# Performance work log

Hardware: AMD Instinct MI355X
Metric: run time of the kernel (lower is better)

Reference implementation:

```python
import jax, jax.numpy as jnp
import numpy as np

B, H, W, D = 4, 64, 64, 384
M, P = 12, 9
DH = D // M             # 32 head dim
DFF = 3 * D             # 1152 FFN hidden
N = H * W               # 4096 queries (single level)


def setup_inputs():
    key = jax.random.key(0)
    ks = jax.random.split(key, 12)
    g = lambda k, s, sc=0.02: jax.random.normal(k, s, jnp.float32) * sc
    return {
        "x": jax.random.normal(ks[0], (B, D, H, W), jnp.float32),
        "qry_masks": jnp.zeros((B, H, W), jnp.float32),
        "so_w": g(ks[1], (M * P * 2, D)), "so_b": g(ks[2], (M * P * 2,)),
        "aw_w": g(ks[3], (M * P, D)), "aw_b": g(ks[4], (M * P,)),
        "vp_w": g(ks[5], (D, D)), "vp_b": jnp.zeros((D,), jnp.float32),
        "op_w": g(ks[6], (D, D)), "op_b": jnp.zeros((D,), jnp.float32),
        "ln1_g": jnp.ones((D,), jnp.float32), "ln1_b": jnp.zeros((D,), jnp.float32),
        "w1": g(ks[7], (DFF, D)), "w2": g(ks[8], (D, DFF)),
        "ln2_g": jnp.ones((D,), jnp.float32), "ln2_b": jnp.zeros((D,), jnp.float32),
        "level_embed": g(ks[9], (1, D), 1.0),
    }


def _layernorm(x, g, b, eps=1e-5):
    mu = x.mean(-1, keepdims=True)
    v = ((x - mu) ** 2).mean(-1, keepdims=True)
    return (x - mu) * jax.lax.rsqrt(v + eps) * g + b


def _sine_pos(mask):
    # mask: [B,H,W] bool. mmdet SinePositionalEncoding(num_feats=D//2, normalize=True)
    not_mask = (~mask).astype(jnp.float32)
    y = jnp.cumsum(not_mask, 1)
    x = jnp.cumsum(not_mask, 2)
    eps, scale = 1e-6, 2.0 * np.pi
    y = y / (y[:, -1:, :] + eps) * scale
    x = x / (x[:, :, -1:] + eps) * scale
    nf = D // 2
    dim_t = 10000.0 ** (2.0 * (jnp.arange(nf) // 2).astype(jnp.float32) / nf)
    px, py = x[..., None] / dim_t, y[..., None] / dim_t

    def interleave(p):
        return jnp.stack([jnp.sin(p[..., 0::2]), jnp.cos(p[..., 1::2])], -1).reshape(p.shape[:-1] + (nf,))

    return jnp.concatenate([interleave(py), interleave(px)], -1)  # [B,H,W,D]


def _bilinear_gather(v, px, py):
    # v: [B,M,HW,DH]; px,py: [B,M,NP] pixel coords (grid_sample align_corners=False, zero pad)
    x0 = jnp.floor(px); y0 = jnp.floor(py)
    lx, ly = px - x0, py - y0
    x0i, y0i = x0.astype(jnp.int32), y0.astype(jnp.int32)
    out = jnp.zeros(v.shape[:2] + (px.shape[-1], v.shape[-1]), v.dtype)
    for dx, dy, wgt in ((0, 0, (1 - lx) * (1 - ly)), (1, 0, lx * (1 - ly)),
                        (0, 1, (1 - lx) * ly), (1, 1, lx * ly)):
        xi, yi = x0i + dx, y0i + dy
        valid = ((xi >= 0) & (xi < W) & (yi >= 0) & (yi < H)).astype(v.dtype)
        idx = jnp.clip(yi, 0, H - 1) * W + jnp.clip(xi, 0, W - 1)
        g = jnp.take_along_axis(v, idx[..., None], axis=2)  # [B,M,NP,DH]
        out = out + (wgt * valid)[..., None] * g
    return out


def _msdeform_attn(q, value_in, ref, mask_flat,
                   so_w, so_b, aw_w, aw_b, vp_w, vp_b, op_w, op_b):
    value = value_in @ vp_w.T + vp_b                      # [B,N,D]
    value = jnp.where(mask_flat[..., None], 0.0, value)
    so = (q @ so_w.T + so_b).reshape(B, N, M, P, 2)       # single level
    aw = jax.nn.softmax((q @ aw_w.T + aw_b).reshape(B, N, M, P), axis=-1)
    norm = jnp.array([W, H], jnp.float32)
    loc = ref[:, :, None, None, :] + so / norm            # [B,N,M,P,2] in [0,1]
    v = value.reshape(B, N, M, DH).transpose(0, 2, 1, 3)  # [B,M,HW,DH]
    px = (loc[..., 0] * W - 0.5).transpose(0, 2, 1, 3).reshape(B, M, N * P)
    py = (loc[..., 1] * H - 0.5).transpose(0, 2, 1, 3).reshape(B, M, N * P)
    sampled = _bilinear_gather(v, px, py).reshape(B, M, N, P, DH)
    out = jnp.einsum('bmnpd,bnmp->bnmd', sampled, aw).reshape(B, N, D)
    return out @ op_w.T + op_b


def reference(x, qry_masks, so_w, so_b, aw_w, aw_b, vp_w, vp_b, op_w, op_b,
              ln1_g, ln1_b, w1, w2, ln2_g, ln2_b, level_embed):
    mask = (qry_masks == 255.0)                           # [B,H,W] bool
    pos = _sine_pos(mask).reshape(B, N, D) + level_embed[0]
    src = x.reshape(B, D, N).transpose(0, 2, 1)           # [B,N,D]
    mask_flat = mask.reshape(B, N)
    gy, gx = jnp.meshgrid((jnp.arange(H, dtype=jnp.float32) + 0.5) / H,
                          (jnp.arange(W, dtype=jnp.float32) + 0.5) / W, indexing='ij')
    ref = jnp.stack([gx.reshape(-1), gy.reshape(-1)], -1)[None]  # [1,N,2] (x,y)
    q = src
    attn = _msdeform_attn(q + pos, q, ref, mask_flat,
                          so_w, so_b, aw_w, aw_b, vp_w, vp_b, op_w, op_b)
    q = _layernorm(q + attn, ln1_g, ln1_b)
    q = _layernorm(q + jax.nn.relu(q @ w1.T) @ w2.T, ln2_g, ln2_b)
    return q.transpose(0, 2, 1).reshape(B, D, H, W)
```

## Files before the change

### kernel.cpp

```cpp
#include <hip/hip_runtime.h>
#include <math.h>

#define Bc   4
#define Hc   64
#define Wc   64
#define Dc   384
#define Nc   4096
#define Mc   12
#define Pc   9
#define DHc  32
#define DFFc 1152
#define BNc  (Bc*Nc)

typedef __attribute__((ext_vector_type(8))) short short8;
typedef __attribute__((ext_vector_type(4))) float floatx4;

__device__ __forceinline__ ushort f2bf(float f) {
    union { float f; unsigned u; } v; v.f = f;
    unsigned r = v.u + 0x7fffu + ((v.u >> 16) & 1u);
    return (ushort)(r >> 16);
}
__device__ __forceinline__ float bf2f(ushort u) {
    union { unsigned u; float f; } v; v.u = (unsigned)u << 16; return v.f;
}

__device__ __forceinline__ void gload_lds16(const void* g, void* l) {
    __builtin_amdgcn_global_load_lds(
        (const __attribute__((address_space(1))) void*)(uintptr_t)g,
        (__attribute__((address_space(3))) void*)(uintptr_t)l,
        16, 0, 0);
}

#define SOW_N  82944
#define AWW_N  41472
#define VPW_N  147456
#define OPW_N  147456
#define W1_N   442368
#define W2_N   442368
#define WTOT   1304064

__global__ void init_kernel(const float* __restrict__ so_w,
                            const float* __restrict__ aw_w,
                            const float* __restrict__ vp_w,
                            const float* __restrict__ op_w,
                            const float* __restrict__ w1,
                            const float* __restrict__ w2,
                            const float* __restrict__ so_b,
                            const float* __restrict__ aw_b,
                            const float* __restrict__ qmask,
                            ushort* __restrict__ out,
                            float* __restrict__ bias_out,
                            float* __restrict__ cum_y,
                            float* __restrict__ cum_x) {
    int i = blockIdx.x * 256 + threadIdx.x;
    if (i < WTOT) {
        float v;
        int j = i;
        if (j < SOW_N) v = so_w[j];
        else if ((j -= SOW_N) < AWW_N) v = aw_w[j];
        else if ((j -= AWW_N) < VPW_N) v = vp_w[j];
        else if ((j -= VPW_N) < OPW_N) v = op_w[j];
        else if ((j -= OPW_N) < W1_N)  v = w1[j];
        else { j -= W1_N; v = w2[j]; }
        out[i] = f2bf(v);
        return;
    }
    int j = i - WTOT;
    if (j < 384) {
        bias_out[j] = (j < 216) ? so_b[j] : (j < 324 ? aw_b[j - 216] : 0.f);
        return;
    }
    int t = j - 384;
    if (t < Bc * Wc) {
        int b = t / Wc, w = t % Wc;
        float run = 0.f;
        for (int h = 0; h < Hc; ++h) {
            run += (qmask[(b * Hc + h) * Wc + w] == 255.0f) ? 0.f : 1.f;
            cum_y[(b * Hc + h) * Wc + w] = run;
        }
    } else if (t < Bc * Wc + Bc * Hc) {
        int t2 = t - Bc * Wc;
        int b = t2 / Hc, h = t2 % Hc;
        float run = 0.f;
        for (int w = 0; w < Wc; ++w) {
            run += (qmask[(b * Hc + h) * Wc + w] == 255.0f) ? 0.f : 1.f;
            cum_x[(b * Hc + h) * Wc + w] = run;
        }
    }
}

__global__ void transpose_pos_kernel(const float* __restrict__ x,
                                     const float* __restrict__ cum_y,
                                     const float* __restrict__ cum_x,
                                     const float* __restrict__ level_embed,
                                     ushort* __restrict__ src_bf,
                                     ushort* __restrict__ qpos_bf) {
    __shared__ float tile[32][33];
    int b  = blockIdx.z;
    int n0 = blockIdx.x * 32, d0 = blockIdx.y * 32;
    int tx = threadIdx.x, ty = threadIdx.y;
    tile[ty][tx] = x[((size_t)b * Dc + (d0 + ty)) * Nc + (n0 + tx)];
    __syncthreads();
    int n = n0 + ty, d = d0 + tx;
    float v = tile[tx][ty];
    size_t oi = ((size_t)b * Nc + n) * Dc + d;
    src_bf[oi] = f2bf(v);
    int h = n >> 6, w = n & 63;
    const float TWO_PI = 6.28318530717958647692f;
    float vy = cum_y[(b * Hc + h) * Wc + w] /
               (cum_y[(b * Hc + (Hc - 1)) * Wc + w] + 1e-6f) * TWO_PI;
    float vx = cum_x[(b * Hc + h) * Wc + w] /
               (cum_x[(b * Hc + h) * Wc + (Wc - 1)] + 1e-6f) * TWO_PI;
    int   i  = (d < 192) ? d : d - 192;
    float vv = (d < 192) ? vy : vx;
    float e   = (float)(i >> 1) * (2.0f / 192.0f);
    float idt = exp2f(e * -13.28771237954945f);
    float ang = vv * idt;
    float pe  = (i & 1) ? __cosf(ang) : __sinf(ang);
    qpos_bf[oi] = f2bf(v + pe + level_embed[d]);
}

template <int KT>
__device__ __forceinline__ void gemm_core(
        const ushort* __restrict__ A, const ushort* __restrict__ Wt,
        const float* __restrict__ bias,
        float* __restrict__ Cf, ushort* __restrict__ Cb,
        int Nout, int relu, const float* __restrict__ qmask,
        ushort* As, ushort* Bs) {
    constexpr int NCH = KT / 32;
    const int tid  = threadIdx.x;
    const int m0   = blockIdx.x * 128;
    const int n0   = blockIdx.y * 128;
    const int lane = tid & 63;
    const int wv   = tid >> 6;
    const int wr   = (wv >> 1) * 64;
    const int wc   = (wv & 1) * 64;
    const int quad = lane >> 4;
    const int lrow = lane & 15;
    const int srow = wv * 32 + (lane >> 2);
    const int scol = (lane & 3) * 8;

    floatx4 acc[4][4];
    #pragma unroll
    for (int i = 0; i < 4; ++i)
        #pragma unroll
        for (int j = 0; j < 4; ++j)
            acc[i][j] = (floatx4)(0.f);

    #pragma unroll
    for (int s = 0; s < 2; ++s) {
        gload_lds16(A  + (size_t)(m0 + srow + s * 16) * KT + scol,
                    As + wv * 1024 + s * 512);
        gload_lds16(Wt + (size_t)(n0 + srow + s * 16) * KT + scol,
                    Bs + wv * 1024 + s * 512);
    }

    for (int c = 0; c < NCH; ++c) {
        const int cur = c & 1;
        __syncthreads();
        if (c + 1 < NCH) {
            const int k0 = (c + 1) * 32;
            #pragma unroll
            for (int s = 0; s < 2; ++s) {
                gload_lds16(A  + (size_t)(m0 + srow + s * 16) * KT + k0 + scol,
                            As + (cur ^ 1) * 4096 + wv * 1024 + s * 512);
                gload_lds16(Wt + (size_t)(n0 + srow + s * 16) * KT + k0 + scol,
                            Bs + (cur ^ 1) * 4096 + wv * 1024 + s * 512);
            }
        }
        short8 afr[4], bfr[4];
        #pragma unroll
        for (int i = 0; i < 4; ++i)
            afr[i] = *(const short8*)(As + cur * 4096 +
                                      (wr + i * 16 + lrow) * 32 + quad * 8);
        #pragma unroll
        for (int j = 0; j < 4; ++j)
            bfr[j] = *(const short8*)(Bs + cur * 4096 +
                                      (wc + j * 16 + lrow) * 32 + quad * 8);
        #pragma unroll
        for (int i = 0; i < 4; ++i)
            #pragma unroll
            for (int j = 0; j < 4; ++j)
                acc[i][j] = __builtin_amdgcn_mfma_f32_16x16x32_bf16(
                    afr[i], bfr[j], acc[i][j], 0, 0, 0);
    }

    float mz[4][4];
    #pragma unroll
    for (int i = 0; i < 4; ++i)
        #pragma unroll
        for (int r = 0; r < 4; ++r) {
            int row = m0 + wr + i * 16 + quad * 4 + r;
            mz[i][r] = (qmask && qmask[row] == 255.0f) ? 0.f : 1.f;
        }

    #pragma unroll
    for (int i = 0; i < 4; ++i) {
        #pragma unroll
        for (int j = 0; j < 4; ++j) {
            int col = n0 + wc + j * 16 + lrow;
            if (col >= Nout) continue;
            float bsv = bias ? bias[col] : 0.f;
            #pragma unroll
            for (int r = 0; r < 4; ++r) {
                int row = m0 + wr + i * 16 + quad * 4 + r;
                float v = acc[i][j][r] + bsv;
                if (relu) v = fmaxf(v, 0.f);
                v *= mz[i][r];
                if (Cf) Cf[(size_t)row * Nout + col] = v;
                if (Cb) Cb[(size_t)row * Nout + col] = f2bf(v);
            }
        }
    }
}

template <int KT>
__global__ __launch_bounds__(256) void gemm_single_kernel(
        const ushort* __restrict__ A, const ushort* __restrict__ Wt,
        const float* __restrict__ bias,
        float* __restrict__ Cf, ushort* __restrict__ Cb,
        int Nout, int relu, const float* __restrict__ qmask) {
    __shared__ ushort As[2 * 128 * 32];
    __shared__ ushort Bs[2 * 128 * 32];
    gemm_core<KT>(A, Wt, bias, Cf, Cb, Nout, relu, qmask, As, Bs);
}

__global__ __launch_bounds__(256) void gemm_dual_kernel(
        const ushort* __restrict__ A0, const ushort* __restrict__ W0,
        const float* __restrict__ b0, float* __restrict__ Cf0,
        const ushort* __restrict__ A1, const ushort* __restrict__ W1,
        const float* __restrict__ b1, ushort* __restrict__ Cb1,
        const float* __restrict__ qmask) {
    __shared__ ushort As[2 * 128 * 32];
    __shared__ ushort Bs[2 * 128 * 32];
    if (blockIdx.z == 0)
        gemm_core<384>(A0, W0, b0, Cf0, nullptr, 384, 0, nullptr, As, Bs);
    else
        gemm_core<384>(A1, W1, b1, nullptr, Cb1, 384, 0, qmask, As, Bs);
}

template <int KT, int MODE>
__global__ __launch_bounds__(512) void gemm_fullrow_kernel(
        const ushort* __restrict__ A, const ushort* __restrict__ Wt,
        const float* __restrict__ bias, const void* __restrict__ resid,
        const float* __restrict__ g, const float* __restrict__ beta,
        float* __restrict__ outf, ushort* __restrict__ outb) {
    constexpr int NCH = KT / 32;
    __shared__ ushort smem[28672];
    __shared__ float eps1[8][64], eps2[8][64];
    __shared__ float mu_l[64], rs_l[64];
    ushort* As = smem;
    ushort* Bs = smem + 4096;
    const int tid  = threadIdx.x;
    const int lane = tid & 63;
    const int wv   = tid >> 6;
    const int quad = lane >> 4;
    const int lrow = lane & 15;
    const int m0   = blockIdx.x * 64;
    const int srow = lane >> 2;
    const int scol = (lane & 3) * 8;

    floatx4 acc[4][3];
    #pragma unroll
    for (int i = 0; i < 4; ++i)
        #pragma unroll
        for (int j = 0; j < 3; ++j)
            acc[i][j] = (floatx4)(0.f);

    if (wv < 4)
        gload_lds16(A + (size_t)(m0 + wv * 16 + srow) * KT + scol,
                    As + wv * 512);
    #pragma unroll
    for (int s = 0; s < 3; ++s)
        gload_lds16(Wt + (size_t)(wv * 48 + s * 16 + srow) * KT + scol,
                    Bs + wv * 1536 + s * 512);

    for (int c = 0; c < NCH; ++c) {
        const int cur = c & 1;
        __syncthreads();
        if (c + 1 < NCH) {
            const int k0 = (c + 1) * 32;
            if (wv < 4)
                gload_lds16(A + (size_t)(m0 + wv * 16 + srow) * KT + k0 + scol,
                            As + (cur ^ 1) * 2048 + wv * 512);
            #pragma unroll
            for (int s = 0; s < 3; ++s)
                gload_lds16(Wt + (size_t)(wv * 48 + s * 16 + srow) * KT + k0 + scol,
                            Bs + (cur ^ 1) * 12288 + wv * 1536 + s * 512);
        }
        short8 afr[4], bfr[3];
        #pragma unroll
        for (int i = 0; i < 4; ++i)
            afr[i] = *(const short8*)(As + cur * 2048 +
                                      (i * 16 + lrow) * 32 + quad * 8);
        #pragma unroll
        for (int j = 0; j < 3; ++j)
            bfr[j] = *(const short8*)(Bs + cur * 12288 +
                                      (wv * 48 + j * 16 + lrow) * 32 + quad * 8);
        #pragma unroll
        for (int i = 0; i < 4; ++i)
            #pragma unroll
            for (int j = 0; j < 3; ++j)
                acc[i][j] = __builtin_amdgcn_mfma_f32_16x16x32_bf16(
                    afr[i], bfr[j], acc[i][j], 0, 0, 0);
    }

    float s1[16], s2[16];
    #pragma unroll
    for (int k = 0; k < 16; ++k) { s1[k] = 0.f; s2[k] = 0.f; }
    #pragma unroll
    for (int i = 0; i < 4; ++i) {
        #pragma unroll
        for (int r = 0; r < 4; ++r) {
            int rl = i * 16 + quad * 4 + r;
            #pragma unroll
            for (int j = 0; j < 3; ++j) {
                int col = wv * 48 + j * 16 + lrow;
                float t = acc[i][j][r];
                if (bias) t += bias[col];
                if (MODE == 0)
                    t += bf2f(((const ushort*)resid)[(size_t)(m0 + rl) * Dc + col]);
                else
                    t += ((const float*)resid)[(size_t)(m0 + rl) * Dc + col];
                acc[i][j][r] = t;
                s1[i * 4 + r] += t;
                s2[i * 4 + r] += t * t;
            }
        }
    }
    #pragma unroll
    for (int m = 1; m < 16; m <<= 1) {
        #pragma unroll
        for (int k = 0; k < 16; ++k) {
            s1[k] += __shfl_xor(s1[k], m);
            s2[k] += __shfl_xor(s2[k], m);
        }
    }
    if (lrow == 0) {
        #pragma unroll
        for (int i = 0; i < 4; ++i)
            #pragma unroll
            for (int r = 0; r < 4; ++r) {
                int rl = i * 16 + quad * 4 + r;
                eps1[wv][rl] = s1[i * 4 + r];
                eps2[wv][rl] = s2[i * 4 + r];
            }
    }
    __syncthreads();
    if (tid < 64) {
        float a1 = 0.f, a2 = 0.f;
        #pragma unroll
        for (int w = 0; w < 8; ++w) { a1 += eps1[w][tid]; a2 += eps2[w][tid]; }
        float mu  = a1 * (1.0f / Dc);
        float var = a2 * (1.0f / Dc) - mu * mu;
        mu_l[tid] = mu;
        rs_l[tid] = rsqrtf(var + 1e-5f);
    }
    __syncthreads();

    #pragma unroll
    for (int i = 0; i < 4; ++i) {
        #pragma unroll
        for (int r = 0; r < 4; ++r) {
            int rl = i * 16 + quad * 4 + r;
            float mu = mu_l[rl], rs = rs_l[rl];
            #pragma unroll
            for (int j = 0; j < 3; ++j) {
                int col = wv * 48 + j * 16 + lrow;
                acc[i][j][r] = (acc[i][j][r] - mu) * rs * g[col] + beta[col];
            }
        }
    }

    if (MODE == 0) {
        #pragma unroll
        for (int i = 0; i < 4; ++i)
            #pragma unroll
            for (int j = 0; j < 3; ++j) {
                int col = wv * 48 + j * 16 + lrow;
                #pragma unroll
                for (int r = 0; r < 4; ++r) {
                    int rl = i * 16 + quad * 4 + r;
                    float v = acc[i][j][r];
                    outf[(size_t)(m0 + rl) * Dc + col] = v;
                    outb[(size_t)(m0 + rl) * Dc + col] = f2bf(v);
                }
            }
    } else {
        float* tile = (float*)smem;
        const int b   = m0 >> 12;
        const int n0r = m0 & 4095;
        #pragma unroll
        for (int gp = 0; gp < 2; ++gp) {
            __syncthreads();
            if ((wv >> 2) == gp) {
                int cbase = (wv & 3) * 48;
                #pragma unroll
                for (int i = 0; i < 4; ++i)
                    #pragma unroll
                    for (int j = 0; j < 3; ++j) {
                        int c = cbase + j * 16 + lrow;
                        #pragma unroll
                        for (int r = 0; r < 4; ++r) {
                            int rl = i * 16 + quad * 4 + r;
                            tile[rl * 193 + c] = acc[i][j][r];
                        }
                    }
            }
            __syncthreads();
            const int row = tid & 63;
            const int cp  = tid >> 6;
            #pragma unroll
            for (int it = 0; it < 24; ++it) {
                int c = it * 8 + cp;
                outf[((size_t)(b * Dc + gp * 192 + c)) * Nc + n0r + row] =
                    tile[row * 193 + c];
            }
        }
    }
}

__global__ __launch_bounds__(256) void deform_attn_kernel(
        const ushort* __restrict__ value_bf, const float* __restrict__ soaw,
        ushort* __restrict__ out) {
    int bid = blockIdx.x;
    int gb  = (bid & 7) * 384 + (bid >> 3);
    int gid = gb * 64 + (threadIdx.x >> 2);
    int l4  = threadIdx.x & 3;
    int m  = gid % Mc;
    int bn = gid / Mc;
    int b  = bn >> 12;
    int n  = bn & 4095;
    int h  = n >> 6, w = n & 63;
    const float* sop = soaw + (size_t)bn * 384 + m * 18;
    const float* lgt = soaw + (size_t)bn * 384 + 216 + m * Pc;
    float awv[Pc];
    float mx = lgt[0];
    #pragma unroll
    for (int i = 1; i < Pc; ++i) mx = fmaxf(mx, lgt[i]);
    float ssum = 0.f;
    #pragma unroll
    for (int i = 0; i < Pc; ++i) { awv[i] = __expf(lgt[i] - mx); ssum += awv[i]; }
    float sinv = 1.f / ssum;
    const ushort* vb = value_bf + ((size_t)b * Nc) * Dc + m * DHc + l4 * 8;
    float acc[8] = {0.f, 0.f, 0.f, 0.f, 0.f, 0.f, 0.f, 0.f};
    #pragma unroll
    for (int p = 0; p < Pc; ++p) {
        float2 so2 = *(const float2*)(sop + p * 2);
        float px = (float)w + so2.x;
        float py = (float)h + so2.y;
        float x0f = floorf(px), y0f = floorf(py);
        float lx = px - x0f, ly = py - y0f;
        int x0 = (int)x0f, y0 = (int)y0f;
        int x1 = x0 + 1,  y1 = y0 + 1;
        float a = awv[p] * sinv;
        float w00 = (1.f - lx) * (1.f - ly) * a;
        float w01 = lx * (1.f - ly) * a;
        float w10 = (1.f - lx) * ly * a;
        float w11 = lx * ly * a;
        bool bx0 = (unsigned)x0 < 64u, bx1 = (unsigned)x1 < 64u;
        bool by0 = (unsigned)y0 < 64u, by1 = (unsigned)y1 < 64u;
        w00 = (bx0 && by0) ? w00 : 0.f;
        w01 = (bx1 && by0) ? w01 : 0.f;
        w10 = (bx0 && by1) ? w10 : 0.f;
        w11 = (bx1 && by1) ? w11 : 0.f;
        int cx0 = min(max(x0, 0), 63), cx1 = min(max(x1, 0), 63);
        int cy0 = min(max(y0, 0), 63), cy1 = min(max(y1, 0), 63);
        uint4 q00 = *(const uint4*)(vb + (size_t)(cy0 * 64 + cx0) * Dc);
        uint4 q01 = *(const uint4*)(vb + (size_t)(cy0 * 64 + cx1) * Dc);
        uint4 q10 = *(const uint4*)(vb + (size_t)(cy1 * 64 + cx0) * Dc);
        uint4 q11 = *(const uint4*)(vb + (size_t)(cy1 * 64 + cx1) * Dc);
        union { unsigned u; float f; } t;
        #define ACC2(word, wg, k)                                   \
            t.u = (word) << 16;         acc[k]     += (wg) * t.f;   \
            t.u = (word) & 0xffff0000u; acc[k + 1] += (wg) * t.f;
        #define ACC8(q, wg) \
            ACC2((q).x, wg, 0) ACC2((q).y, wg, 2) ACC2((q).z, wg, 4) ACC2((q).w, wg, 6)
        ACC8(q00, w00) ACC8(q01, w01) ACC8(q10, w10) ACC8(q11, w11)
        #undef ACC8
        #undef ACC2
    }
    short8 o;
    #pragma unroll
    for (int k = 0; k < 8; ++k) o[k] = (short)f2bf(acc[k]);
    *(short8*)(out + (size_t)bn * Dc + m * DHc + l4 * 8) = o;
}

extern "C" void kernel_launch(void* const* d_in, const int* in_sizes, int n_in,
                              void* d_out, int out_size, void* d_ws, size_t ws_size,
                              hipStream_t stream) {
    (void)in_sizes; (void)n_in; (void)out_size; (void)ws_size;
    const float* x      = (const float*)d_in[0];
    const float* qmask  = (const float*)d_in[1];
    const float* so_w   = (const float*)d_in[2];
    const float* so_b   = (const float*)d_in[3];
    const float* aw_w   = (const float*)d_in[4];
    const float* aw_b   = (const float*)d_in[5];
    const float* vp_w   = (const float*)d_in[6];
    const float* vp_b   = (const float*)d_in[7];
    const float* op_w   = (const float*)d_in[8];
    const float* op_b   = (const float*)d_in[9];
    const float* ln1_g  = (const float*)d_in[10];
    const float* ln1_b  = (const float*)d_in[11];
    const float* w1     = (const float*)d_in[12];
    const float* w2     = (const float*)d_in[13];
    const float* ln2_g  = (const float*)d_in[14];
    const float* ln2_b  = (const float*)d_in[15];
    const float* lvl    = (const float*)d_in[16];
    float* out = (float*)d_out;

    float*  ws       = (float*)d_ws;
    float*  q1_f     = ws;
    ushort* src_bf   = (ushort*)(q1_f + 6291456);
    ushort* qpos_bf  = src_bf + 6291456;
    ushort* value_bf = qpos_bf + 6291456;
    ushort* hbuf_bf  = value_bf + 6291456;
    float*  soaw_f   = (float*)hbuf_bf;
    ushort* wbuf     = hbuf_bf + 18874368;
    float*  soaw_bias= (float*)(wbuf + 1304064);
    float*  cum_y    = soaw_bias + 384;
    float*  cum_x    = cum_y + 16384;

    const ushort* soaw_wb = wbuf;
    const ushort* vp_wb = soaw_wb + SOW_N + AWW_N;
    const ushort* op_wb = vp_wb + VPW_N;
    const ushort* w1_b  = op_wb + OPW_N;
    const ushort* w2_b  = w1_b + W1_N;

    init_kernel<<<(WTOT + 384 + 512 + 255) / 256, 256, 0, stream>>>(
        so_w, aw_w, vp_w, op_w, w1, w2, so_b, aw_b, qmask,
        wbuf, soaw_bias, cum_y, cum_x);
    transpose_pos_kernel<<<dim3(Nc / 32, Dc / 32, Bc), dim3(32, 32), 0, stream>>>(
        x, cum_y, cum_x, lvl, src_bf, qpos_bf);
    gemm_dual_kernel<<<dim3(BNc / 128, 3, 2), 256, 0, stream>>>(
        qpos_bf, soaw_wb, soaw_bias, soaw_f,
        src_bf, vp_wb, vp_b, value_bf, qmask);
    deform_attn_kernel<<<(BNc * Mc) / 64, 256, 0, stream>>>(
        value_bf, soaw_f, qpos_bf);
    gemm_fullrow_kernel<384, 0><<<BNc / 64, 512, 0, stream>>>(
        qpos_bf, op_wb, op_b, src_bf, ln1_g, ln1_b, q1_f, qpos_bf);
    gemm_single_kernel<384><<<dim3(BNc / 128, 9), 256, 0, stream>>>(
        qpos_bf, w1_b, nullptr, nullptr, hbuf_bf, DFFc, 1, nullptr);
    gemm_fullrow_kernel<1152, 1><<<BNc / 64, 512, 0, stream>>>(
        hbuf_bf, w2_b, nullptr, q1_f, ln2_g, ln2_b, out, nullptr);
}
```

Measured before the change: 265.0 us.

## Deepen fullrow GEMM pipeline, split cumsum kernel, remap deform-attn blocks

The full-row GEMM+LayerNorm kernel moves from a double-buffered LDS pipeline to a 4-buffer ring with three chunks in flight. It uses explicit vmcnt waits and a raw barrier to hide global-load latency better, at the cost of more LDS and lower occupancy. Mask cumsums move from serial per-thread loops over global memory into a separate LDS-based kernel. Deform attention blocks are remapped so each block covers one image row for a single (batch, head), which should improve locality of the value gathers.

```diff
diff --git a/kernel.cpp b/kernel.cpp
--- a/kernel.cpp
+++ b/kernel.cpp
@@ -47,11 +47,8 @@
                             const float* __restrict__ w2,
                             const float* __restrict__ so_b,
                             const float* __restrict__ aw_b,
-                            const float* __restrict__ qmask,
                             ushort* __restrict__ out,
-                            float* __restrict__ bias_out,
-                            float* __restrict__ cum_y,
-                            float* __restrict__ cum_x) {
+                            float* __restrict__ bias_out) {
     int i = blockIdx.x * 256 + threadIdx.x;
     if (i < WTOT) {
         float v;
@@ -68,24 +65,43 @@
     int j = i - WTOT;
     if (j < 384) {
         bias_out[j] = (j < 216) ? so_b[j] : (j < 324 ? aw_b[j - 216] : 0.f);
-        return;
-    }
-    int t = j - 384;
-    if (t < Bc * Wc) {
-        int b = t / Wc, w = t % Wc;
+    }
+}
+
+__global__ __launch_bounds__(256) void cumsum_kernel(
+        const float* __restrict__ qmask,
+        float* __restrict__ cum_y, float* __restrict__ cum_x) {
+    __shared__ float nm[64 * 65];
+    __shared__ float ot[64 * 65];
+    int b = blockIdx.x;
+    int t = threadIdx.x;
+    const float* qm = qmask + b * 4096;
+    #pragma unroll
+    for (int k = 0; k < 16; ++k) {
+        int idx = t + k * 256;
+        nm[(idx >> 6) * 65 + (idx & 63)] = (qm[idx] == 255.0f) ? 0.f : 1.f;
+    }
+    __syncthreads();
+    if (t < 64) {
         float run = 0.f;
-        for (int h = 0; h < Hc; ++h) {
-            run += (qmask[(b * Hc + h) * Wc + w] == 255.0f) ? 0.f : 1.f;
-            cum_y[(b * Hc + h) * Wc + w] = run;
-        }
-    } else if (t < Bc * Wc + Bc * Hc) {
-        int t2 = t - Bc * Wc;
-        int b = t2 / Hc, h = t2 % Hc;
+        for (int h = 0; h < 64; ++h) { run += nm[h * 65 + t]; ot[h * 65 + t] = run; }
+    }
+    __syncthreads();
+    #pragma unroll
+    for (int k = 0; k < 16; ++k) {
+        int idx = t + k * 256;
+        cum_y[b * 4096 + idx] = ot[(idx >> 6) * 65 + (idx & 63)];
+    }
+    __syncthreads();
+    if (t < 64) {
         float run = 0.f;
-        for (int w = 0; w < Wc; ++w) {
-            run += (qmask[(b * Hc + h) * Wc + w] == 255.0f) ? 0.f : 1.f;
-            cum_x[(b * Hc + h) * Wc + w] = run;
-        }
+        for (int w = 0; w < 64; ++w) { run += nm[t * 65 + w]; ot[t * 65 + w] = run; }
+    }
+    __syncthreads();
+    #pragma unroll
+    for (int k = 0; k < 16; ++k) {
+        int idx = t + k * 256;
+        cum_x[b * 4096 + idx] = ot[(idx >> 6) * 65 + (idx & 63)];
     }
 }
 
@@ -246,11 +262,10 @@
         const float* __restrict__ g, const float* __restrict__ beta,
         float* __restrict__ outf, ushort* __restrict__ outb) {
     constexpr int NCH = KT / 32;
-    __shared__ ushort smem[28672];
+    __shared__ ushort As[4 * 2048];
+    __shared__ ushort Bs[4 * 12288];
     __shared__ float eps1[8][64], eps2[8][64];
     __shared__ float mu_l[64], rs_l[64];
-    ushort* As = smem;
-    ushort* Bs = smem + 4096;
     const int tid  = threadIdx.x;
     const int lane = tid & 63;
     const int wv   = tid >> 6;
@@ -267,35 +282,45 @@
         for (int j = 0; j < 3; ++j)
             acc[i][j] = (floatx4)(0.f);
 
-    if (wv < 4)
-        gload_lds16(A + (size_t)(m0 + wv * 16 + srow) * KT + scol,
-                    As + wv * 512);
-    #pragma unroll
-    for (int s = 0; s < 3; ++s)
-        gload_lds16(Wt + (size_t)(wv * 48 + s * 16 + srow) * KT + scol,
-                    Bs + wv * 1536 + s * 512);
-
+#define STAGE_CHUNK(c, buf)                                                   \
+    {   const int k0_ = (c) * 32;                                             \
+        if (wv < 4)                                                           \
+            gload_lds16(A + (size_t)(m0 + wv * 16 + srow) * KT + k0_ + scol,  \
+                        As + (buf) * 2048 + wv * 512);                        \
+        _Pragma("unroll")                                                     \
+        for (int s_ = 0; s_ < 3; ++s_)                                        \
+            gload_lds16(Wt + (size_t)(wv * 48 + s_ * 16 + srow) * KT + k0_ + scol, \
+                        Bs + (buf) * 12288 + wv * 1536 + s_ * 512);           \
+    }
+
+    STAGE_CHUNK(0, 0)
+    STAGE_CHUNK(1, 1)
+    STAGE_CHUNK(2, 2)
+
+    #pragma unroll
     for (int c = 0; c < NCH; ++c) {
-        const int cur = c & 1;
-        __syncthreads();
-        if (c + 1 < NCH) {
-            const int k0 = (c + 1) * 32;
-            if (wv < 4)
-                gload_lds16(A + (size_t)(m0 + wv * 16 + srow) * KT + k0 + scol,
-                            As + (cur ^ 1) * 2048 + wv * 512);
-            #pragma unroll
-            for (int s = 0; s < 3; ++s)
-                gload_lds16(Wt + (size_t)(wv * 48 + s * 16 + srow) * KT + k0 + scol,
-                            Bs + (cur ^ 1) * 12288 + wv * 1536 + s * 512);
-        }
+        const int rem = (NCH - 1 - c) >= 2 ? 2 : (NCH - 1 - c);
+        if (wv < 4) {
+            if (rem == 2)      asm volatile("s_waitcnt vmcnt(8)" ::: "memory");
+            else if (rem == 1) asm volatile("s_waitcnt vmcnt(4)" ::: "memory");
+            else               asm volatile("s_waitcnt vmcnt(0)" ::: "memory");
+        } else {
+            if (rem == 2)      asm volatile("s_waitcnt vmcnt(6)" ::: "memory");
+            else if (rem == 1) asm volatile("s_waitcnt vmcnt(3)" ::: "memory");
+            else               asm volatile("s_waitcnt vmcnt(0)" ::: "memory");
+        }
+        __builtin_amdgcn_s_barrier();
+        __builtin_amdgcn_sched_barrier(0);
+        if (c + 3 < NCH) { STAGE_CHUNK(c + 3, (c + 3) & 3) }
+        const int buf = c & 3;
         short8 afr[4], bfr[3];
         #pragma unroll
         for (int i = 0; i < 4; ++i)
-            afr[i] = *(const short8*)(As + cur * 2048 +
+            afr[i] = *(const short8*)(As + buf * 2048 +
                                       (i * 16 + lrow) * 32 + quad * 8);
         #pragma unroll
         for (int j = 0; j < 3; ++j)
-            bfr[j] = *(const short8*)(Bs + cur * 12288 +
+            bfr[j] = *(const short8*)(Bs + buf * 12288 +
                                       (wv * 48 + j * 16 + lrow) * 32 + quad * 8);
         #pragma unroll
         for (int i = 0; i < 4; ++i)
@@ -304,6 +329,7 @@
                 acc[i][j] = __builtin_amdgcn_mfma_f32_16x16x32_bf16(
                     afr[i], bfr[j], acc[i][j], 0, 0, 0);
     }
+#undef STAGE_CHUNK
 
     float s1[16], s2[16];
     #pragma unroll
@@ -329,11 +355,11 @@
         }
     }
     #pragma unroll
-    for (int m = 1; m < 16; m <<= 1) {
+    for (int mm = 1; mm < 16; mm <<= 1) {
         #pragma unroll
         for (int k = 0; k < 16; ++k) {
-            s1[k] += __shfl_xor(s1[k], m);
-            s2[k] += __shfl_xor(s2[k], m);
+            s1[k] += __shfl_xor(s1[k], mm);
+            s2[k] += __shfl_xor(s2[k], mm);
         }
     }
     if (lrow == 0) {
@@ -387,7 +413,7 @@
                 }
             }
     } else {
-        float* tile = (float*)smem;
+        float* tile = (float*)Bs;
         const int b   = m0 >> 12;
         const int n0r = m0 & 4095;
         #pragma unroll
@@ -423,15 +449,15 @@
 __global__ __launch_bounds__(256) void deform_attn_kernel(
         const ushort* __restrict__ value_bf, const float* __restrict__ soaw,
         ushort* __restrict__ out) {
-    int bid = blockIdx.x;
-    int gb  = (bid & 7) * 384 + (bid >> 3);
-    int gid = gb * 64 + (threadIdx.x >> 2);
-    int l4  = threadIdx.x & 3;
-    int m  = gid % Mc;
-    int bn = gid / Mc;
-    int b  = bn >> 12;
-    int n  = bn & 4095;
-    int h  = n >> 6, w = n & 63;
+    int bid   = blockIdx.x;
+    int slice = bid % 48;
+    int h     = bid / 48;
+    int m  = slice % Mc;
+    int b  = slice / Mc;
+    int w  = threadIdx.x >> 2;
+    int l4 = threadIdx.x & 3;
+    int n  = (h << 6) | w;
+    int bn = b * Nc + n;
     const float* sop = soaw + (size_t)bn * 384 + m * 18;
     const float* lgt = soaw + (size_t)bn * 384 + 216 + m * Pc;
     float awv[Pc];
@@ -527,15 +553,15 @@
     const ushort* w1_b  = op_wb + OPW_N;
     const ushort* w2_b  = w1_b + W1_N;
 
-    init_kernel<<<(WTOT + 384 + 512 + 255) / 256, 256, 0, stream>>>(
-        so_w, aw_w, vp_w, op_w, w1, w2, so_b, aw_b, qmask,
-        wbuf, soaw_bias, cum_y, cum_x);
+    init_kernel<<<(WTOT + 384 + 255) / 256, 256, 0, stream>>>(
+        so_w, aw_w, vp_w, op_w, w1, w2, so_b, aw_b, wbuf, soaw_bias);
+    cumsum_kernel<<<Bc, 256, 0, stream>>>(qmask, cum_y, cum_x);
     transpose_pos_kernel<<<dim3(Nc / 32, Dc / 32, Bc), dim3(32, 32), 0, stream>>>(
         x, cum_y, cum_x, lvl, src_bf, qpos_bf);
     gemm_dual_kernel<<<dim3(BNc / 128, 3, 2), 256, 0, stream>>>(
         qpos_bf, soaw_wb, soaw_bias, soaw_f,
         src_bf, vp_wb, vp_b, value_bf, qmask);
-    deform_attn_kernel<<<(BNc * Mc) / 64, 256, 0, stream>>>(
+    deform_attn_kernel<<<3072, 256, 0, stream>>>(
         value_bf, soaw_f, qpos_bf);
     gemm_fullrow_kernel<384, 0><<<BNc / 64, 512, 0, stream>>>(
         qpos_bf, op_wb, op_b, src_bf, ln1_g, ln1_b, q1_f, qpos_bf);
```

New measurement: 269.7 us. No clear change (+1.8%).
